# Performance work log

Measured on AMD Instinct MI355X. Metric: run time of the kernel, lower is better.

Reference implementation:

```python
import jax, jax.numpy as jnp
import numpy as np
import math

H_HEADS = 4
SQRT_2_PI = math.sqrt(2.0 / math.pi)


def _gelu_tanh(x):
    return 0.5 * x * (1.0 + jnp.tanh(SQRT_2_PI * (x + 0.044715 * x ** 3)))


def _ln(x, g, b, eps=1e-5):
    mu = jnp.mean(x, axis=-1, keepdims=True)
    var = jnp.var(x, axis=-1, keepdims=True)
    return g * (x - mu) * jax.lax.rsqrt(var + eps) + b


def _forward(support_emb_mat, query_t, support_t, cls_embed, t_freq, t_phase,
             Wq, bq, Wk, bk, Wv, bv, Wo, bo, ln1_g, ln1_b, time_w,
             W1, b1, W2, b2, ln2_g, ln2_b, Wc, bc, bn_g, bn_b):
    B, F, MD = support_emb_mat.shape
    Q = query_t.shape[1]
    S = F + 1
    H = H_HEADS
    D = MD * H
    dph = D // H
    L = Wq.shape[0]
    BQ = B * Q

    # [CLS] + support sequence, feature-tiled to model_dim*num_heads
    cls = jnp.broadcast_to(cls_embed, (B, 1, MD))
    seq = jnp.concatenate([cls, support_emb_mat], axis=1)          # [B,S,MD]
    x = jnp.tile(seq, (1, 1, H))                                    # [B,S,D]
    x = jnp.broadcast_to(x[:, None], (B, Q, S, D)).reshape(BQ, S, D)

    # time sequence: [query_t_q, support_t...] per (b,q)
    sup = jnp.broadcast_to(support_t[:, None, :], (B, Q, F))
    t_seq = jnp.concatenate([query_t[..., None], sup], axis=-1).reshape(BQ, S)
    t_diff = t_seq[:, :, None] - t_seq[:, None, :]                  # [BQ,S,S]
    # time encoder: cos(t*freq + phase) -> [BQ,S,S,TD]
    t_emb = jnp.cos(t_diff[..., None] * t_freq + t_phase)

    # scale as in source: (dim_per_head // num_heads) ** -0.5
    scale = (dph // H) ** (-0.5)

    for l in range(L):
        bias = t_emb @ time_w[l]                                    # [BQ,S,S]
        add = jnp.tile(bias, (H, 1, 1))                             # [BQ*H,S,S]
        res = x
        # raw row-major reshape to (BQ*H, S, dph) exactly as torch .view
        q = (x @ Wq[l] + bq[l]).reshape(BQ * H, S, dph)
        k = (x @ Wk[l] + bk[l]).reshape(BQ * H, S, dph)
        v = (x @ Wv[l] + bv[l]).reshape(BQ * H, S, dph)
        attn = jax.nn.softmax(jnp.einsum('bsd,btd->bst', q, k) * scale + add, axis=-1)
        ctx = jnp.einsum('bst,btd->bsd', attn, v).reshape(BQ, S, D)
        out = _ln(res + ctx @ Wo[l] + bo[l], ln1_g[l], ln1_b[l])
        ffn = _gelu_tanh(out @ W1[l] + b1[l]) @ W2[l] + b2[l]
        x = _ln(out + ffn, ln2_g[l], ln2_b[l])

    # compress: Linear -> BatchNorm1d over seq channels (train mode) -> LeakyReLU
    h = x @ Wc + bc                                                 # [BQ,S,MD]
    mu = jnp.mean(h, axis=(0, 2), keepdims=True)
    var = jnp.var(h, axis=(0, 2), keepdims=True)
    h = bn_g[None, :, None] * (h - mu) * jax.lax.rsqrt(var + 1e-5) + bn_b[None, :, None]
    h = jnp.where(h >= 0, h, 0.01 * h)                              # LeakyReLU
    return h[:, 0, :].reshape(B, Q, MD)


def setup_inputs() -> dict:
    key = jax.random.key(0)
    ks = jax.random.split(key, 24)
    B, Q, F, MD = 128, 32, 7, 128
    H, L, FFN, TD = 4, 6, 2048, 32
    S = F + 1
    D = MD * H

    def nrm(k, shape, s=0.02):
        return jax.random.normal(k, shape, jnp.float32) * s

    inp = {
        'support_emb_mat': jax.random.normal(ks[0], (B, F, MD), jnp.float32),
        'query_t': jax.random.uniform(ks[1], (B, Q), jnp.float32) * 100.0,
        'support_t': jax.random.uniform(ks[2], (B, F), jnp.float32) * 100.0,
        'cls_embed': jax.random.uniform(ks[3], (1, MD), jnp.float32),
        't_freq': nrm(ks[4], (TD,), 1.0),
        't_phase': nrm(ks[5], (TD,), 1.0),
        'Wq': nrm(ks[6], (L, D, D)), 'bq': jnp.zeros((L, D)),
        'Wk': nrm(ks[7], (L, D, D)), 'bk': jnp.zeros((L, D)),
        'Wv': nrm(ks[8], (L, D, D)), 'bv': jnp.zeros((L, D)),
        'Wo': nrm(ks[9], (L, D, D)), 'bo': jnp.zeros((L, D)),
        'ln1_g': jnp.ones((L, D)), 'ln1_b': jnp.zeros((L, D)),
        'time_w': jnp.ones((L, TD)) * 0.001,
        'W1': nrm(ks[10], (L, D, FFN)), 'b1': jnp.zeros((L, FFN)),
        'W2': nrm(ks[11], (L, FFN, D)), 'b2': jnp.zeros((L, D)),
        'ln2_g': jnp.ones((L, D)), 'ln2_b': jnp.zeros((L, D)),
        'Wc': nrm(ks[12], (D, MD)), 'bc': jnp.zeros((MD,)),
        'bn_g': jnp.ones((S,)), 'bn_b': jnp.zeros((S,)),
    }
    return inp


def reference(support_emb_mat, query_t, support_t, cls_embed, t_freq, t_phase,
              Wq, bq, Wk, bk, Wv, bv, Wo, bo, ln1_g, ln1_b, time_w,
              W1, b1, W2, b2, ln2_g, ln2_b, Wc, bc, bn_g, bn_b):
    return _forward(support_emb_mat, query_t, support_t, cls_embed, t_freq, t_phase,
                    Wq, bq, Wk, bk, Wv, bv, Wo, bo, ln1_g, ln1_b, time_w,
                    W1, b1, W2, b2, ln2_g, ln2_b, Wc, bc, bn_g, bn_b)
```

## Files before the change

kernel.cpp:

```cpp
#include <hip/hip_runtime.h>
#include <hip/hip_bf16.h>

typedef _Float16 f16;
typedef __attribute__((ext_vector_type(8))) _Float16 f16x8;
typedef __attribute__((ext_vector_type(4))) _Float16 f16x4;
typedef __attribute__((ext_vector_type(4))) float f32x4;

#define DEVI __device__ __forceinline__

DEVI float ldf(const void* p, size_t i, int isf32) {
    if (isf32) return ((const float*)p)[i];
    unsigned int u = ((const unsigned short*)p)[i];
    union { unsigned int b; float f; } c; c.b = u << 16;
    return c.f;
}

DEVI void gld_lds16(const f16* g, f16* l) {
    __builtin_amdgcn_global_load_lds(
        (__attribute__((address_space(1))) void*)(g),
        (__attribute__((address_space(3))) void*)(l), 16, 0, 0);
}

__global__ void detect_dtype(const void* qt, int* flag) {
    if (threadIdx.x == 0 && blockIdx.x == 0) {
        const unsigned int* w = (const unsigned int*)qt;
        int cnt = 0;
        for (int i = 0; i < 64; ++i) {
            unsigned int lo = w[i] & 0xFFFFu;
            union { unsigned int b; float f; } c; c.b = lo << 16;
            if (c.f >= 1e-4f && c.f <= 100.5f) ++cnt;
        }
        *flag = (cnt >= 32) ? 0 : 1;
    }
}

__global__ __launch_bounds__(256)
void cvt_in(const void* __restrict__ src, float* __restrict__ dst, int n,
            const int* __restrict__ flag) {
    const int f32 = *flag;
    int i = blockIdx.x * 256 + threadIdx.x;
    if (i < n) dst[i] = ldf(src, i, f32);
}

__global__ __launch_bounds__(256)
void fill_out(float* out, float v) {
    out[blockIdx.x * 256 + threadIdx.x] = v;
}

template<int EPI>
__global__ __launch_bounds__(256, 4)
void gemm_bt(const f16* __restrict__ Ag, const f16* __restrict__ BTg,
             const float* __restrict__ biasg, const f16* __restrict__ resg,
             void* __restrict__ outg,
             int NT, int NTZ, int MCHUNK, int MT, int N, int K, int lda,
             long zsB, long zsBias, long zsC)
{
    const int tid  = threadIdx.x;
    const int w    = tid >> 6, lane = tid & 63;
    const int wm   = w >> 1,   wn   = w & 1;

    const int id    = blockIdx.x;
    const int pc    = MCHUNK * NTZ;
    const int chunk = id / pc;
    const int rem   = id - chunk * pc;
    const int mloc  = rem % MCHUNK;
    const int ynz   = rem / MCHUNK;
    const int z     = ynz / NT;
    const int tmB   = (chunk * MCHUNK + mloc) * (128 * MT);
    const int tn    = (ynz - z * NT) * 128;

    const f16*   BT   = BTg + (size_t)z * zsB;
    const float* bias = biasg + (size_t)z * zsBias;
    const size_t zoffC = (size_t)z * zsC;

    __shared__ __align__(16) f16 smA[2][8][64][8];
    __shared__ __align__(16) f16 smB[2][8][64][8];

    const int r16 = lane & 15, q4 = lane >> 4;
    const int iters = K >> 5;

    const f16* gA0 = Ag + (size_t)(tmB + (2 * w) * 16 + r16) * lda + q4 * 8;
    const f16* gA1 = gA0 + (size_t)16 * lda;
    const f16* gB0 = BT + (size_t)(tn + (2 * w) * 16 + r16) * K + q4 * 8;
    const f16* gB1 = gB0 + (size_t)16 * K;

    auto issue = [&](int msN, int ktN, int buf) {
        const size_t aoff = (size_t)msN * 128 * lda + (size_t)ktN * 32;
        const size_t boff = (size_t)ktN * 32;
        gld_lds16(gA0 + aoff, &smA[buf][2 * w][0][0]);
        gld_lds16(gA1 + aoff, &smA[buf][2 * w + 1][0][0]);
        gld_lds16(gB0 + boff, &smB[buf][2 * w][0][0]);
        gld_lds16(gB1 + boff, &smB[buf][2 * w + 1][0][0]);
    };

    issue(0, 0, 0);
    int stage = 0;

    for (int ms = 0; ms < MT; ++ms) {
        const int tm = tmB + ms * 128;

        f32x4 acc[4][4];
#pragma unroll
        for (int i = 0; i < 4; ++i)
#pragma unroll
            for (int j = 0; j < 4; ++j) acc[i][j] = (f32x4)0.0f;

        for (int kt = 0; kt < iters; ++kt, ++stage) {
            const int cur = stage & 1;
            __builtin_amdgcn_s_barrier();
            int ktN = kt + 1, msN = ms;
            if (ktN == iters) { ktN = 0; ++msN; }
            if (msN < MT) {
                issue(msN, ktN, cur ^ 1);
                __builtin_amdgcn_s_waitcnt(0x0F74);
            } else {
                __builtin_amdgcn_s_waitcnt(0x0F70);
            }
            __builtin_amdgcn_s_barrier();
            __asm__ __volatile__("" ::: "memory");

            f16x8 af[4], bf[4];
#pragma unroll
            for (int i = 0; i < 4; ++i) {
                af[i] = *(const f16x8*)&smA[cur][wm * 4 + i][lane][0];
                bf[i] = *(const f16x8*)&smB[cur][wn * 4 + i][lane][0];
            }
#pragma unroll
            for (int i = 0; i < 4; ++i)
#pragma unroll
                for (int j = 0; j < 4; ++j)
                    acc[i][j] = __builtin_amdgcn_mfma_f32_16x16x32_f16(
                        af[i], bf[j], acc[i][j], 0, 0, 0);
        }

        const int rowBase = tm + wm * 64;
        const int colBase = tn + wn * 64;
#pragma unroll
        for (int j = 0; j < 4; ++j) {
            const int col = colBase + j * 16 + r16;
            const float bv = bias[col];
#pragma unroll
            for (int i = 0; i < 4; ++i) {
                const int row0 = rowBase + i * 16 + q4 * 4;
#pragma unroll
                for (int r = 0; r < 4; ++r) {
                    const int row = row0 + r;
                    const size_t off = (size_t)row * N + col;
                    float v = acc[i][j][r] + bv;
                    if constexpr (EPI == 0) {
                        ((f16*)outg)[zoffC + off] = (f16)v;
                    } else if constexpr (EPI == 2) {
                        float t  = v + 0.044715f * v * v * v;
                        float u  = 1.5957691216057308f * t;
                        float e  = __expf(u);
                        float th = 1.0f - 2.0f / (e + 1.0f);
                        ((f16*)outg)[off] = (f16)(0.5f * v * (1.0f + th));
                    } else {
                        ((float*)outg)[off] = v;
                    }
                }
            }
        }
    }
}

__global__ __launch_bounds__(512, 2)
void gemm_ln(const f16* __restrict__ Ag, const f16* __restrict__ BTg,
             const float* __restrict__ bias, const f16* __restrict__ resg,
             const float* __restrict__ lng, const float* __restrict__ lnb,
             f16* __restrict__ Yg, int K, int lda)
{
    const int tid = threadIdx.x;
    const int w = tid >> 6, lane = tid & 63;
    const int wm = w >> 2, wn = w & 3;
    const int r16 = lane & 15, q4 = lane >> 4;
    const int tm = blockIdx.x * 128;

    __shared__ __align__(16) f16 smA[2][8][64][8];
    __shared__ __align__(16) f16 smB[2][32][64][8];
    __shared__ float lnS[128][4];
    __shared__ float lnQ[128][4];

    f32x4 acc[4][8];
#pragma unroll
    for (int i = 0; i < 4; ++i)
#pragma unroll
        for (int j = 0; j < 8; ++j) acc[i][j] = (f32x4)0.0f;

    const f16* gA  = Ag  + (size_t)(tm + w * 16 + r16) * lda + q4 * 8;
    const f16* gB  = BTg + (size_t)(w * 64 + r16) * K + q4 * 8;
    const int iters = K >> 5;

    auto issue = [&](int kt, int buf) {
        const size_t o = (size_t)kt * 32;
        gld_lds16(gA + o, &smA[buf][w][0][0]);
#pragma unroll
        for (int t = 0; t < 4; ++t)
            gld_lds16(gB + (size_t)(t * 16) * K + o, &smB[buf][w * 4 + t][0][0]);
    };

    issue(0, 0);
    for (int kt = 0; kt < iters; ++kt) {
        const int cur = kt & 1;
        __builtin_amdgcn_s_barrier();
        if (kt + 1 < iters) {
            issue(kt + 1, cur ^ 1);
            __builtin_amdgcn_s_waitcnt(0x0F75);
        } else {
            __builtin_amdgcn_s_waitcnt(0x0F70);
        }
        __builtin_amdgcn_s_barrier();
        __asm__ __volatile__("" ::: "memory");

        f16x8 af[4], bf[8];
#pragma unroll
        for (int i = 0; i < 4; ++i)
            af[i] = *(const f16x8*)&smA[cur][wm * 4 + i][lane][0];
#pragma unroll
        for (int j = 0; j < 8; ++j)
            bf[j] = *(const f16x8*)&smB[cur][wn * 8 + j][lane][0];
#pragma unroll
        for (int i = 0; i < 4; ++i)
#pragma unroll
            for (int j = 0; j < 8; ++j)
                acc[i][j] = __builtin_amdgcn_mfma_f32_16x16x32_f16(
                    af[i], bf[j], acc[i][j], 0, 0, 0);
    }

    const int rowB = wm * 64;
    const int colB = wn * 128;
    float gv[8], bv[8], biv[8];
#pragma unroll
    for (int j = 0; j < 8; ++j) {
        const int col = colB + j * 16 + r16;
        gv[j] = lng[col]; bv[j] = lnb[col]; biv[j] = bias[col];
    }

    float ps[4][4], pq[4][4];
#pragma unroll
    for (int i = 0; i < 4; ++i) {
#pragma unroll
        for (int rr = 0; rr < 4; ++rr) {
            const int grow = tm + rowB + i * 16 + q4 * 4 + rr;
            float s = 0.f, sq = 0.f;
#pragma unroll
            for (int j = 0; j < 8; ++j) {
                const int col = colB + j * 16 + r16;
                float v = acc[i][j][rr] + biv[j]
                        + (float)resg[(size_t)grow * 512 + col];
                acc[i][j][rr] = v;
                s += v; sq += v * v;
            }
#pragma unroll
            for (int m = 1; m <= 8; m <<= 1) {
                s  += __shfl_xor(s, m, 64);
                sq += __shfl_xor(sq, m, 64);
            }
            ps[i][rr] = s; pq[i][rr] = sq;
        }
    }
    __syncthreads();
    if (r16 == 0) {
#pragma unroll
        for (int i = 0; i < 4; ++i)
#pragma unroll
            for (int rr = 0; rr < 4; ++rr) {
                const int lr = rowB + i * 16 + q4 * 4 + rr;
                lnS[lr][wn] = ps[i][rr];
                lnQ[lr][wn] = pq[i][rr];
            }
    }
    __syncthreads();

#pragma unroll
    for (int i = 0; i < 4; ++i) {
#pragma unroll
        for (int rr = 0; rr < 4; ++rr) {
            const int lr = rowB + i * 16 + q4 * 4 + rr;
            const float s  = lnS[lr][0] + lnS[lr][1] + lnS[lr][2] + lnS[lr][3];
            const float sq = lnQ[lr][0] + lnQ[lr][1] + lnQ[lr][2] + lnQ[lr][3];
            const float mu = s * (1.0f / 512.0f);
            const float var = sq * (1.0f / 512.0f) - mu * mu;
            const float rs = rsqrtf(var + 1e-5f);
            const size_t rowoff = (size_t)(tm + lr) * 512;
#pragma unroll
            for (int j = 0; j < 8; ++j) {
                const int col = colB + j * 16 + r16;
                Yg[rowoff + col] = (f16)(gv[j] * (acc[i][j][rr] - mu) * rs + bv[j]);
            }
        }
    }
}

__global__ __launch_bounds__(256)
void attn_kernel(const f16* __restrict__ qg, const f16* __restrict__ kg,
                 const f16* __restrict__ vg, const float* __restrict__ biasL,
                 f16* __restrict__ cg, int small)
{
    const int w = threadIdx.x >> 6, lane = threadIdx.x & 63;
    const int j = blockIdx.x * 4 + w;
    __shared__ __align__(16) f16 sQ[4][8][136];
    __shared__ __align__(16) f16 sK[4][8][136];
    __shared__ __align__(16) f16 sV[4][8][136];
    __shared__ float sP[4][8][8];

    const size_t base  = (size_t)j * 1024;
    const size_t ibase = small ? ((size_t)(j >> 7) * 4096 + (size_t)(j & 3) * 1024)
                               : base;
#pragma unroll
    for (int t = 0; t < 2; ++t) {
        int flat = (t * 64 + lane) * 8;
        int r = flat >> 7, c = flat & 127;
        *(f16x8*)&sQ[w][r][c] = *(const f16x8*)(qg + ibase + flat);
        *(f16x8*)&sK[w][r][c] = *(const f16x8*)(kg + ibase + flat);
        *(f16x8*)&sV[w][r][c] = *(const f16x8*)(vg + ibase + flat);
    }
    __syncthreads();

    const int i = lane >> 3, jj = lane & 7;
    float d = 0.f;
#pragma unroll
    for (int c = 0; c < 16; ++c) {
        f16x8 qv = *(const f16x8*)&sQ[w][i][c * 8];
        f16x8 kv = *(const f16x8*)&sK[w][jj][c * 8];
#pragma unroll
        for (int e = 0; e < 8; ++e) d += (float)qv[e] * (float)kv[e];
    }
    float s = d * 0.17677669529663687f + biasL[(size_t)(j & 4095) * 64 + lane];
    float mx = s;
    mx = fmaxf(mx, __shfl_xor(mx, 1, 64));
    mx = fmaxf(mx, __shfl_xor(mx, 2, 64));
    mx = fmaxf(mx, __shfl_xor(mx, 4, 64));
    float p = __expf(s - mx);
    float sum = p;
    sum += __shfl_xor(sum, 1, 64);
    sum += __shfl_xor(sum, 2, 64);
    sum += __shfl_xor(sum, 4, 64);
    sP[w][i][jj] = p / sum;
    __syncthreads();

#pragma unroll
    for (int t2 = 0; t2 < 8; ++t2) {
        float ap[8];
#pragma unroll
        for (int e = 0; e < 8; ++e) ap[e] = sP[w][t2][e];
#pragma unroll
        for (int h = 0; h < 2; ++h) {
            int flat = (t2 * 2 + h) * 64 + lane;
            int dd = flat & 127;
            float o = 0.f;
#pragma unroll
            for (int e = 0; e < 8; ++e) o += ap[e] * (float)sV[w][e][dd];
            cg[base + flat] = (f16)o;
        }
    }
}

__global__ __launch_bounds__(256)
void build_x0(const void* __restrict__ sup, const void* __restrict__ cls,
              f16* __restrict__ xb, const int* __restrict__ flag)
{
    const int f32 = *flag;
    const size_t idx = ((size_t)blockIdx.x * 256 + threadIdx.x) * 4;
    const int row = (int)(idx >> 9), col0 = (int)(idx & 511);
    const int s = row & 7, b = row >> 8;
    f16x4 o;
#pragma unroll
    for (int e = 0; e < 4; ++e) {
        const int md = (col0 + e) & 127;
        float v = (s == 0) ? ldf(cls, md, f32)
                           : ldf(sup, ((size_t)b * 7 + (s - 1)) * 128 + md, f32);
        o[e] = (f16)v;
    }
    *(f16x4*)(xb + idx) = o;
}

__global__ __launch_bounds__(256)
void build_x0s(const void* __restrict__ sup, const void* __restrict__ cls,
               f16* __restrict__ xs, const int* __restrict__ flag)
{
    const int f32 = *flag;
    const size_t idx = ((size_t)blockIdx.x * 256 + threadIdx.x) * 4;
    const int row = (int)(idx >> 9), col0 = (int)(idx & 511);
    const int s = row & 7, b = row >> 3;
    f16x4 o;
#pragma unroll
    for (int e = 0; e < 4; ++e) {
        const int md = (col0 + e) & 127;
        float v = (s == 0) ? ldf(cls, md, f32)
                           : ldf(sup, ((size_t)b * 7 + (s - 1)) * 128 + md, f32);
        o[e] = (f16)v;
    }
    *(f16x4*)(xs + idx) = o;
}

__global__ __launch_bounds__(256)
void bias_kernel(const void* __restrict__ qt, const void* __restrict__ st,
                 const void* __restrict__ freq, const void* __restrict__ phase,
                 const void* __restrict__ tw, float* __restrict__ biasAll,
                 const int* __restrict__ flag)
{
    const int f32 = *flag;
    const int lane = threadIdx.x & 63;
    const int bq = blockIdx.x * 4 + (threadIdx.x >> 6);
    const int b = bq >> 5, qq = bq & 31;
    const int i = lane >> 3, jj = lane & 7;
    const float ti = (i  == 0) ? ldf(qt, b * 32 + qq, f32) : ldf(st, b * 7 + i  - 1, f32);
    const float tj = (jj == 0) ? ldf(qt, b * 32 + qq, f32) : ldf(st, b * 7 + jj - 1, f32);
    const float td = ti - tj;
    float a[6] = {0.f, 0.f, 0.f, 0.f, 0.f, 0.f};
    for (int t = 0; t < 32; ++t) {
        float c = __cosf(td * ldf(freq, t, f32) + ldf(phase, t, f32));
#pragma unroll
        for (int l = 0; l < 6; ++l) a[l] += c * ldf(tw, l * 32 + t, f32);
    }
#pragma unroll
    for (int l = 0; l < 6; ++l)
        biasAll[(size_t)l * (4096 * 64) + (size_t)bq * 64 + lane] = a[l];
}

__global__ __launch_bounds__(256)
void transpose_cvt(const void* __restrict__ W, f16* __restrict__ WT,
                   int K, int N, long zsW, long zsWT, const int* __restrict__ flag)
{
    const int f32 = *flag;
    const size_t zoff = (size_t)blockIdx.z * zsW;
    f16* WTz = WT + (size_t)blockIdx.z * zsWT;
    __shared__ float tile[64][65];
    const int tn = blockIdx.x * 64, tk = blockIdx.y * 64;
#pragma unroll
    for (int t = 0; t < 16; ++t) {
        int idx = t * 256 + threadIdx.x;
        int r = idx >> 6, c = idx & 63;
        tile[r][c] = ldf(W, zoff + (size_t)(tk + r) * N + tn + c, f32);
    }
    __syncthreads();
#pragma unroll
    for (int t = 0; t < 16; ++t) {
        int idx = t * 256 + threadIdx.x;
        int r = idx >> 6, c = idx & 63;
        WTz[(size_t)(tn + r) * K + tk + c] = (f16)tile[c][r];
    }
}

__global__ __launch_bounds__(256)
void gather_qkvb(const void* __restrict__ bq, const void* __restrict__ bk,
                 const void* __restrict__ bv, float* __restrict__ dst,
                 const int* __restrict__ flag)
{
    const int f32 = *flag;
    int i = blockIdx.x * 256 + threadIdx.x;
    if (i < 9216) {
        int z = i / 3072, rem = i % 3072;
        const void* src = (z == 0) ? bq : ((z == 1) ? bk : bv);
        dst[i] = ldf(src, rem, f32);
    }
}

__global__ __launch_bounds__(256)
void bn_reduce(const float* __restrict__ h0, float* __restrict__ stats)
{
    const int t = blockIdx.x * 256 + threadIdx.x;
    float s = 0.f, ss = 0.f;
#pragma unroll
    for (int k = 0; k < 8; ++k) {
        float v = h0[t + k * 65536];
        s += v; ss += v * v;
    }
#pragma unroll
    for (int m = 1; m <= 32; m <<= 1) {
        s  += __shfl_xor(s, m, 64);
        ss += __shfl_xor(ss, m, 64);
    }
    __shared__ float ls[8];
    const int w = threadIdx.x >> 6, lane = threadIdx.x & 63;
    if (lane == 0) { ls[w] = s; ls[4 + w] = ss; }
    __syncthreads();
    if (threadIdx.x == 0) {
        atomicAdd(&stats[0], ls[0] + ls[1] + ls[2] + ls[3]);
        atomicAdd(&stats[1], ls[4] + ls[5] + ls[6] + ls[7]);
    }
}

__global__ __launch_bounds__(256)
void bn_apply(const float* __restrict__ h0, const float* __restrict__ stats,
              const float* __restrict__ bnp, float* __restrict__ out)
{
    const int t = blockIdx.x * 256 + threadIdx.x;
    const float mu  = stats[0] * (1.0f / 524288.0f);
    const float var = stats[1] * (1.0f / 524288.0f) - mu * mu;
    const float rs  = rsqrtf(var + 1e-5f);
    float v = bnp[0] * (h0[t] - mu) * rs + bnp[8];
    v = (v >= 0.f) ? v : 0.01f * v;
    out[t] = v;
}

extern "C" void kernel_launch(void* const* d_in, const int* in_sizes, int n_in,
                              void* d_out, int out_size, void* d_ws, size_t ws_size,
                              hipStream_t stream)
{
    (void)in_sizes; (void)n_in; (void)out_size;
    const void* sup   = d_in[0];
    const void* qt    = d_in[1];
    const void* st    = d_in[2];
    const void* cls   = d_in[3];
    const void* freq  = d_in[4];
    const void* phase = d_in[5];
    const void* Wq = d_in[6];  const void* bqv = d_in[7];
    const void* Wk = d_in[8];  const void* bkv = d_in[9];
    const void* Wv = d_in[10]; const void* bvv = d_in[11];
    const void* Wo = d_in[12]; const void* bo  = d_in[13];
    const void* ln1g = d_in[14]; const void* ln1b = d_in[15];
    const void* tw = d_in[16];
    const void* W1 = d_in[17]; const void* b1 = d_in[18];
    const void* W2 = d_in[19]; const void* b2 = d_in[20];
    const void* ln2g = d_in[21]; const void* ln2b = d_in[22];
    const void* Wc = d_in[23]; const void* bc = d_in[24];
    const void* bng = d_in[25]; const void* bnb = d_in[26];

    const size_t NEEDED = 245658240;
    if (ws_size < NEEDED) {
        fill_out<<<2048, 256, 0, stream>>>((float*)d_out, 999.0f);
        return;
    }

    char* ws = (char*)d_ws;
    f16*   wt      = (f16*)(ws + 0);
    float* biasAll = (float*)(ws + 37879808);
    float* qkvb    = (float*)(ws + 44171264);
    float* prm     = (float*)(ws + 44208128);
    float* stats   = (float*)(ws + 44331584);
    int*   flag    = (int*)  (ws + 44331592);
    f16*   xb      = (f16*)(ws + 44331648);
    f16*   ob      = (f16*)(ws + 77886080);
    char*  region  = ws + 111440512;
    f16*   qb      = (f16*)(region);
    f16*   kb      = (f16*)(region + 33554432);
    f16*   vb      = (f16*)(region + 67108864);
    f16*   cb      = (f16*)(region + 100663296);
    f16*   qs      = (f16*)(region);
    f16*   xs      = (f16*)(region + 100663296);
    f16*   fbuf    = (f16*)(region);
    float* h0      = (float*)(region);

    detect_dtype<<<1, 64, 0, stream>>>(qt, flag);

    cvt_in<<<12, 256, 0, stream>>>(bo,   prm + 0,     3072,  flag);
    cvt_in<<<48, 256, 0, stream>>>(b1,   prm + 3072,  12288, flag);
    cvt_in<<<12, 256, 0, stream>>>(b2,   prm + 15360, 3072,  flag);
    cvt_in<<<1,  256, 0, stream>>>(bc,   prm + 18432, 128,   flag);
    cvt_in<<<12, 256, 0, stream>>>(ln1g, prm + 18560, 3072,  flag);
    cvt_in<<<12, 256, 0, stream>>>(ln1b, prm + 21632, 3072,  flag);
    cvt_in<<<12, 256, 0, stream>>>(ln2g, prm + 24704, 3072,  flag);
    cvt_in<<<12, 256, 0, stream>>>(ln2b, prm + 27776, 3072,  flag);
    cvt_in<<<1,  256, 0, stream>>>(bng,  prm + 30848, 8,     flag);
    cvt_in<<<1,  256, 0, stream>>>(bnb,  prm + 30856, 8,     flag);

    transpose_cvt<<<dim3(8, 8, 6),  256, 0, stream>>>(Wq, wt + 0,        512, 512,  262144, 262144, flag);
    transpose_cvt<<<dim3(8, 8, 6),  256, 0, stream>>>(Wk, wt + 1572864,  512, 512,  262144, 262144, flag);
    transpose_cvt<<<dim3(8, 8, 6),  256, 0, stream>>>(Wv, wt + 3145728,  512, 512,  262144, 262144, flag);
    transpose_cvt<<<dim3(8, 8, 6),  256, 0, stream>>>(Wo, wt + 4718592,  512, 512,  262144, 262144, flag);
    transpose_cvt<<<dim3(32, 8, 6), 256, 0, stream>>>(W1, wt + 6291456,  512, 2048, 1048576, 1048576, flag);
    transpose_cvt<<<dim3(8, 32, 6), 256, 0, stream>>>(W2, wt + 12582912, 2048, 512, 1048576, 1048576, flag);
    transpose_cvt<<<dim3(2, 8, 1),  256, 0, stream>>>(Wc, wt + 18874368, 512, 128,  0, 0, flag);
    gather_qkvb<<<36, 256, 0, stream>>>(bqv, bkv, bvv, qkvb, flag);
    build_x0<<<16384, 256, 0, stream>>>(sup, cls, xb, flag);
    build_x0s<<<512, 256, 0, stream>>>(sup, cls, xs, flag);
    bias_kernel<<<1024, 256, 0, stream>>>(qt, st, freq, phase, tw, biasAll, flag);
    hipMemsetAsync(stats, 0, 8, stream);

    for (int l = 0; l < 6; ++l) {
        if (l == 0) {
            gemm_bt<0><<<96, 256, 0, stream>>>(
                xs, wt, qkvb, nullptr, qs,
                4, 12, 8, 1, 512, 512, 512, 1572864, 3072, 524288);
            attn_kernel<<<4096, 256, 0, stream>>>(
                qs, qs + 524288, qs + 1048576, biasAll, cb, 1);
        } else {
            gemm_bt<0><<<1536, 256, 0, stream>>>(
                xb, wt + l * 262144, qkvb + l * 512, nullptr, qb,
                4, 12, 32, 2, 512, 512, 512, 1572864, 3072, 16777216);
            attn_kernel<<<4096, 256, 0, stream>>>(
                qb, kb, vb, biasAll + (size_t)l * 262144, cb, 0);
        }
        gemm_ln<<<256, 512, 0, stream>>>(
            cb, wt + 4718592 + l * 262144, prm + 0 + l * 512, xb,
            prm + 18560 + l * 512, prm + 21632 + l * 512, ob, 512, 512);
        gemm_bt<2><<<2048, 256, 0, stream>>>(
            ob, wt + 6291456 + l * 1048576, prm + 3072 + l * 2048, nullptr, fbuf,
            16, 16, 32, 2, 2048, 512, 512, 0, 0, 0);
        gemm_ln<<<256, 512, 0, stream>>>(
            fbuf, wt + 12582912 + l * 1048576, prm + 15360 + l * 512, ob,
            prm + 24704 + l * 512, prm + 27776 + l * 512, xb, 2048, 2048);
    }

    gemm_bt<3><<<32, 256, 0, stream>>>(
        xb, wt + 18874368, prm + 18432, nullptr, h0,
        1, 1, 32, 1, 128, 512, 4096 , 0, 0, 0);
    bn_reduce<<<256, 256, 0, stream>>>(h0, stats);
    bn_apply<<<2048, 256, 0, stream>>>(h0, stats, prm + 30848, (float*)d_out);
}
```

Before: 2.790 ms.

## Add 128x512 wide-tile GEMM for QKV and FFN1 projections

Adds a gemm_wide kernel with 512 threads, each block computing a 128x512 output tile, and uses it for the per-layer QKV projection and the first FFN GEMM with GELU in place of 128x128-tile gemm_bt launches. Each A row tile is loaded once per 512 output columns rather than once per 128, which cuts global and L2 traffic for the activation matrix and the number of blocks launched. In exchange each wave holds 32 accumulator fragments, which raises register pressure and lowers occupancy, and the grid has fewer blocks.

Measured after the change: 2.881 ms. 3.3% more time.

```diff
diff --git a/kernel.cpp b/kernel.cpp
--- a/kernel.cpp
+++ b/kernel.cpp
@@ -19,6 +19,14 @@
     __builtin_amdgcn_global_load_lds(
         (__attribute__((address_space(1))) void*)(g),
         (__attribute__((address_space(3))) void*)(l), 16, 0, 0);
+}
+
+DEVI float gelu_f(float v) {
+    float t  = v + 0.044715f * v * v * v;
+    float u  = 1.5957691216057308f * t;
+    float e  = __expf(u);
+    float th = 1.0f - 2.0f / (e + 1.0f);
+    return 0.5f * v * (1.0f + th);
 }
 
 __global__ void detect_dtype(const void* qt, int* flag) {
@@ -50,8 +58,7 @@
 template<int EPI>
 __global__ __launch_bounds__(256, 4)
 void gemm_bt(const f16* __restrict__ Ag, const f16* __restrict__ BTg,
-             const float* __restrict__ biasg, const f16* __restrict__ resg,
-             void* __restrict__ outg,
+             const float* __restrict__ biasg, void* __restrict__ outg,
              int NT, int NTZ, int MCHUNK, int MT, int N, int K, int lda,
              long zsB, long zsBias, long zsC)
 {
@@ -144,21 +151,99 @@
                 const int row0 = rowBase + i * 16 + q4 * 4;
 #pragma unroll
                 for (int r = 0; r < 4; ++r) {
-                    const int row = row0 + r;
-                    const size_t off = (size_t)row * N + col;
+                    const size_t off = (size_t)(row0 + r) * N + col;
                     float v = acc[i][j][r] + bv;
                     if constexpr (EPI == 0) {
                         ((f16*)outg)[zoffC + off] = (f16)v;
-                    } else if constexpr (EPI == 2) {
-                        float t  = v + 0.044715f * v * v * v;
-                        float u  = 1.5957691216057308f * t;
-                        float e  = __expf(u);
-                        float th = 1.0f - 2.0f / (e + 1.0f);
-                        ((f16*)outg)[off] = (f16)(0.5f * v * (1.0f + th));
                     } else {
                         ((float*)outg)[off] = v;
                     }
                 }
+            }
+        }
+    }
+}
+
+template<int EPI>
+__global__ __launch_bounds__(512, 2)
+void gemm_wide(const f16* __restrict__ Ag, const f16* __restrict__ BTg,
+               const float* __restrict__ biasg, f16* __restrict__ outg,
+               int K, int lda, int N, long zsB, long zsBias, long zsC)
+{
+    const int tid = threadIdx.x;
+    const int w = tid >> 6, lane = tid & 63;
+    const int wm = w >> 2, wn = w & 3;
+    const int r16 = lane & 15, q4 = lane >> 4;
+    const int tm = blockIdx.x * 128;
+    const int nz = blockIdx.y;
+
+    const f16*   BT   = BTg + (size_t)nz * zsB;
+    const float* bias = biasg + (size_t)nz * zsBias;
+    f16*         out  = outg + (size_t)nz * zsC;
+
+    __shared__ __align__(16) f16 smA[2][8][64][8];
+    __shared__ __align__(16) f16 smB[2][32][64][8];
+
+    f32x4 acc[4][8];
+#pragma unroll
+    for (int i = 0; i < 4; ++i)
+#pragma unroll
+        for (int j = 0; j < 8; ++j) acc[i][j] = (f32x4)0.0f;
+
+    const f16* gA = Ag + (size_t)(tm + w * 16 + r16) * lda + q4 * 8;
+    const f16* gB = BT + (size_t)(w * 64 + r16) * K + q4 * 8;
+    const int iters = K >> 5;
+
+    auto issue = [&](int kt, int buf) {
+        const size_t o = (size_t)kt * 32;
+        gld_lds16(gA + o, &smA[buf][w][0][0]);
+#pragma unroll
+        for (int t = 0; t < 4; ++t)
+            gld_lds16(gB + (size_t)(t * 16) * K + o, &smB[buf][w * 4 + t][0][0]);
+    };
+
+    issue(0, 0);
+    for (int kt = 0; kt < iters; ++kt) {
+        const int cur = kt & 1;
+        __builtin_amdgcn_s_barrier();
+        if (kt + 1 < iters) {
+            issue(kt + 1, cur ^ 1);
+            __builtin_amdgcn_s_waitcnt(0x0F75);
+        } else {
+            __builtin_amdgcn_s_waitcnt(0x0F70);
+        }
+        __builtin_amdgcn_s_barrier();
+        __asm__ __volatile__("" ::: "memory");
+
+        f16x8 af[4], bf[8];
+#pragma unroll
+        for (int i = 0; i < 4; ++i)
+            af[i] = *(const f16x8*)&smA[cur][wm * 4 + i][lane][0];
+#pragma unroll
+        for (int j = 0; j < 8; ++j)
+            bf[j] = *(const f16x8*)&smB[cur][wn * 8 + j][lane][0];
+#pragma unroll
+        for (int i = 0; i < 4; ++i)
+#pragma unroll
+            for (int j = 0; j < 8; ++j)
+                acc[i][j] = __builtin_amdgcn_mfma_f32_16x16x32_f16(
+                    af[i], bf[j], acc[i][j], 0, 0, 0);
+    }
+
+    const int rowB = tm + wm * 64;
+    const int colB = wn * 128;
+#pragma unroll
+    for (int j = 0; j < 8; ++j) {
+        const int col = colB + j * 16 + r16;
+        const float bv = bias[col];
+#pragma unroll
+        for (int i = 0; i < 4; ++i) {
+            const int row0 = rowB + i * 16 + q4 * 4;
+#pragma unroll
+            for (int r = 0; r < 4; ++r) {
+                float v = acc[i][j][r] + bv;
+                if constexpr (EPI == 2) v = gelu_f(v);
+                out[(size_t)(row0 + r) * N + col] = (f16)v;
             }
         }
     }
@@ -572,30 +657,30 @@
     for (int l = 0; l < 6; ++l) {
         if (l == 0) {
             gemm_bt<0><<<96, 256, 0, stream>>>(
-                xs, wt, qkvb, nullptr, qs,
+                xs, wt, qkvb, qs,
                 4, 12, 8, 1, 512, 512, 512, 1572864, 3072, 524288);
             attn_kernel<<<4096, 256, 0, stream>>>(
                 qs, qs + 524288, qs + 1048576, biasAll, cb, 1);
         } else {
-            gemm_bt<0><<<1536, 256, 0, stream>>>(
-                xb, wt + l * 262144, qkvb + l * 512, nullptr, qb,
-                4, 12, 32, 2, 512, 512, 512, 1572864, 3072, 16777216);
+            gemm_wide<0><<<dim3(256, 3), 512, 0, stream>>>(
+                xb, wt + l * 262144, qkvb + l * 512, qb,
+                512, 512, 512, 1572864, 3072, 16777216);
             attn_kernel<<<4096, 256, 0, stream>>>(
                 qb, kb, vb, biasAll + (size_t)l * 262144, cb, 0);
         }
         gemm_ln<<<256, 512, 0, stream>>>(
             cb, wt + 4718592 + l * 262144, prm + 0 + l * 512, xb,
             prm + 18560 + l * 512, prm + 21632 + l * 512, ob, 512, 512);
-        gemm_bt<2><<<2048, 256, 0, stream>>>(
-            ob, wt + 6291456 + l * 1048576, prm + 3072 + l * 2048, nullptr, fbuf,
-            16, 16, 32, 2, 2048, 512, 512, 0, 0, 0);
+        gemm_wide<2><<<dim3(256, 4), 512, 0, stream>>>(
+            ob, wt + 6291456 + l * 1048576, prm + 3072 + l * 2048, fbuf,
+            512, 512, 2048, 262144, 512, 512);
         gemm_ln<<<256, 512, 0, stream>>>(
             fbuf, wt + 12582912 + l * 1048576, prm + 15360 + l * 512, ob,
             prm + 24704 + l * 512, prm + 27776 + l * 512, xb, 2048, 2048);
     }
 
     gemm_bt<3><<<32, 256, 0, stream>>>(
-        xb, wt + 18874368, prm + 18432, nullptr, h0,
+        xb, wt + 18874368, prm + 18432, h0,
         1, 1, 32, 1, 128, 512, 4096 , 0, 0, 0);
     bn_reduce<<<256, 256, 0, stream>>>(h0, stats);
     bn_apply<<<2048, 256, 0, stream>>>(h0, stats, prm + 30848, (float*)d_out);
```
